# Kernel optimization log

Hardware: AMD Instinct MI355X
Metric: run time of the kernel (lower is better)

## Reference

```python
import jax, jax.numpy as jnp
import numpy as np

D = 64          # embed_dim == latent dim
T = 200         # diffusion_steps, timestep_respacing='' -> full 200 reverse steps
B, L = 8192, 100
N_ITEMS = 100000


def setup_inputs() -> dict:
    key = jax.random.key(0)
    ks = jax.random.split(key, 16)

    def lin(k, i, o):
        return (jax.random.normal(k, (i, o), jnp.float32) / np.sqrt(i)).astype(jnp.float32)

    item_seq = jax.random.randint(ks[0], (B, L), 0, N_ITEMS)
    item_emb = jax.random.normal(ks[1], (N_ITEMS, D), jnp.float32) * 0.02
    item_emb = item_emb.at[0].set(0.0)  # padding_idx=0
    return {
        'item_seq': item_seq,
        'item_emb': item_emb,
        'W_enc1': lin(ks[2], D, 256), 'b_enc1': jnp.zeros((256,), jnp.float32),
        'W_enc2': lin(ks[3], 256, 2 * D), 'b_enc2': jnp.zeros((2 * D,), jnp.float32),
        'W_in': lin(ks[4], D, D), 'b_in': jnp.zeros((D,), jnp.float32),
        'W_t': lin(ks[5], D, D), 'b_t': jnp.zeros((D,), jnp.float32),
        'W_c': lin(ks[6], D, D), 'b_c': jnp.zeros((D,), jnp.float32),
        'W_out': lin(ks[7], D, D), 'b_out': jnp.zeros((D,), jnp.float32),
    }


def _schedule():
    # improved-diffusion linear schedule
    scale = 1000.0 / T
    betas = jnp.linspace(scale * 1e-4, scale * 0.02, T, dtype=jnp.float32)
    alphas = 1.0 - betas
    acp = jnp.cumprod(alphas)
    acp_prev = jnp.concatenate([jnp.ones((1,), jnp.float32), acp[:-1]])
    sqrt_recip = jnp.sqrt(1.0 / acp)
    sqrt_recipm1 = jnp.sqrt(1.0 / acp - 1.0)
    post_var = betas * (1.0 - acp_prev) / (1.0 - acp)
    post_logvar = jnp.log(jnp.concatenate([post_var[1:2], post_var[1:]]))  # clipped
    coef1 = betas * jnp.sqrt(acp_prev) / (1.0 - acp)
    coef2 = (1.0 - acp_prev) * jnp.sqrt(alphas) / (1.0 - acp)
    return sqrt_recip, sqrt_recipm1, post_logvar, coef1, coef2


def reference(item_seq, item_emb, W_enc1, b_enc1, W_enc2, b_enc2,
              W_in, b_in, W_t, b_t, W_c, b_c, W_out, b_out):
    # ---- pooled VAE encoder (eval mode: dropout = identity, z = mu) ----
    seq = item_emb[item_seq]                                   # [B, L, D] gather
    cnt = jnp.sum(item_seq != 0, axis=1, keepdims=True).astype(seq.dtype)
    pooled = jnp.sum(seq, axis=1) / jnp.sqrt(cnt)              # [B, D]
    h = jax.nn.relu(pooled @ W_enc1 + b_enc1)
    enc = h @ W_enc2 + b_enc2                                  # [B, 2D]
    mu, logvar = jnp.split(enc, 2, axis=-1)
    z = mu                                                     # eval reparameterize

    # ---- ScoreNet: eps-prediction MLP conditioned on x_start and sinusoidal t ----
    half = D // 2
    freqs = jnp.exp(-jnp.log(10000.0) * jnp.arange(half, dtype=jnp.float32) / half)

    def scorenet(x, t_float, cond):
        ang = t_float * freqs                                  # [D/2]
        temb = jnp.concatenate([jnp.cos(ang), jnp.sin(ang)])   # [D]
        hh = jax.nn.silu(x @ W_in + b_in + (temb @ W_t + b_t) + cond @ W_c + b_c)
        return hh @ W_out + b_out                              # eps, [B, D]

    # ---- p_sample_loop (FIXED_SMALL variance, clip_denoised=True) ----
    sqrt_recip, sqrt_recipm1, post_logvar, coef1, coef2 = _schedule()
    x_init = jax.random.normal(jax.random.key(1), z.shape, z.dtype)
    noise_key = jax.random.key(2)

    def step(x, t):
        eps = scorenet(x, t.astype(jnp.float32), z)
        x0 = jnp.clip(sqrt_recip[t] * x - sqrt_recipm1[t] * eps, -1.0, 1.0)
        mean = coef1[t] * x0 + coef2[t] * x
        noise = jax.random.normal(jax.random.fold_in(noise_key, t), x.shape, x.dtype)
        sigma = jnp.where(t > 0, jnp.exp(0.5 * post_logvar[t]), 0.0)
        return mean + sigma * noise, None

    sample, _ = jax.lax.scan(step, x_init, jnp.arange(T - 1, -1, -1))
    return sample
```

## Files before the change

### kernel.cpp

```cpp
#include <hip/hip_runtime.h>
#include <cstdint>


#define DEVI __device__ __forceinline__

typedef __attribute__((ext_vector_type(8))) short short8;
typedef __attribute__((ext_vector_type(4))) float f32x4;

DEVI void threefry2x32(uint32_t k0, uint32_t k1, uint32_t x0, uint32_t x1,
                       uint32_t &o0, uint32_t &o1)
{
  const uint32_t ks2 = k0 ^ k1 ^ 0x1BD11BDAu;
  x0 += k0; x1 += k1;
#define TFR(r) { x0 += x1; x1 = __builtin_rotateleft32(x1, r); x1 ^= x0; }
  TFR(13u) TFR(15u) TFR(26u) TFR(6u)   x0 += k1;  x1 += ks2 + 1u;
  TFR(17u) TFR(29u) TFR(16u) TFR(24u)  x0 += ks2; x1 += k0 + 2u;
  TFR(13u) TFR(15u) TFR(26u) TFR(6u)   x0 += k0;  x1 += k1 + 3u;
  TFR(17u) TFR(29u) TFR(16u) TFR(24u)  x0 += k1;  x1 += ks2 + 4u;
  TFR(13u) TFR(15u) TFR(26u) TFR(6u)   x0 += ks2; x1 += k0 + 5u;
#undef TFR
  o0 = x0; o1 = x1;
}

DEVI uint32_t jax_random_bits32(uint32_t k0, uint32_t k1, uint32_t j)
{
  uint32_t a, b;
  threefry2x32(k0, k1, 0u, j, a, b);
  return a ^ b;
}

DEVI float jax_bits_to_normal(uint32_t bits)
{
  const float LO = -0.99999994f;
  float f = __uint_as_float((bits >> 9) | 0x3f800000u) - 1.0f;
  float u = fmaxf(LO, f * 2.0f + LO);
  float w = -__logf((1.0f - u) * (1.0f + u));
  float p;
  if (w < 5.0f) {
    w = w - 2.5f;
    p =              2.81022636e-08f;
    p = fmaf(p, w,   3.43273939e-07f);
    p = fmaf(p, w,  -3.5233877e-06f);
    p = fmaf(p, w,  -4.39150654e-06f);
    p = fmaf(p, w,   0.00021858087f);
    p = fmaf(p, w,  -0.00125372503f);
    p = fmaf(p, w,  -0.00417768164f);
    p = fmaf(p, w,   0.246640727f);
    p = fmaf(p, w,   1.50140941f);
  } else {
    w = sqrtf(w) - 3.0f;
    p =             -0.000200214257f;
    p = fmaf(p, w,   0.000100950558f);
    p = fmaf(p, w,   0.00134934322f);
    p = fmaf(p, w,  -0.00367342844f);
    p = fmaf(p, w,   0.00573950773f);
    p = fmaf(p, w,  -0.0076224613f);
    p = fmaf(p, w,   0.00943887047f);
    p = fmaf(p, w,   1.00167406f);
    p = fmaf(p, w,   2.83297682f);
  }
  return 1.41421356237f * (p * u);
}

DEVI short bf16_hi_trunc(float x) { return (short)(__float_as_uint(x) >> 16); }
DEVI float bf16_to_f32(short h)
{
  return __uint_as_float(((uint32_t)(unsigned short)h) << 16);
}
DEVI void split_bf16(float x, short &h, short &l)
{
  h = bf16_hi_trunc(x);
  float r = x - bf16_to_f32(h);
  l = bf16_hi_trunc(r);
}

DEVI short8 ld_frag16(const short* p)
{
  union { int4 v; short8 s; } u;
  u.v = *(const int4*)p;
  return u.s;
}

__global__ __launch_bounds__(256)
void k_poolprep(const int* __restrict__ seq, const float* __restrict__ emb,
                float* __restrict__ pooled,
                const float* __restrict__ Wt, const float* __restrict__ bt,
                const float* __restrict__ bin, float* __restrict__ tpb,
                float* __restrict__ sched)
{
  if (blockIdx.x < 2048u) {
    const int lane = threadIdx.x & 63;
    const int r    = blockIdx.x * 4 + (threadIdx.x >> 6);
    const int* row = seq + r * 100;
    float s = 0.f;
    int cnt = 0;
    for (int l = 0; l < 100; ++l) {
      int id = row[l];
      cnt += (id != 0);
      s += emb[id * 64 + lane];
    }
    pooled[r * 64 + lane] = s / sqrtf((float)cnt);
  } else {
    __shared__ float temb[64];
    const int t = blockIdx.x - 2048;
    const int d = threadIdx.x;
    if (d < 64) {
      const float lg = logf(10000.0f);
      int i = d & 31;
      float fr  = expf((-lg * (float)i) / 32.0f);
      float ang = (float)t * fr;
      temb[d] = (d < 32) ? cosf(ang) : sinf(ang);
      if (d == 0) {
        const float start = (float)(5.0 * 1e-4);
        const float stop  = (float)(5.0 * 0.02);
        const float delta = stop - start;
        float prod = 1.f, acp_prev = 1.f, beta = 0.f, alpha = 1.f;
        for (int i2 = 0; i2 <= t; ++i2) {
          beta  = start + ((float)i2 * delta) / 199.0f;
          alpha = 1.0f - beta;
          acp_prev = prod;
          prod = prod * alpha;
        }
        float acp = prod;
        float om  = 1.0f - acp;
        sched[t * 8 + 0] = sqrtf(1.0f / acp);
        sched[t * 8 + 1] = sqrtf(1.0f / acp - 1.0f);
        sched[t * 8 + 2] = beta * sqrtf(acp_prev) / om;
        sched[t * 8 + 3] = (1.0f - acp_prev) * sqrtf(alpha) / om;
        float pv = beta * (1.0f - acp_prev) / om;
        sched[t * 8 + 4] = (t > 0) ? sqrtf(pv) : 0.0f;
        uint32_t fk0, fk1;
        threefry2x32(0u, 2u, 0u, (uint32_t)t, fk0, fk1);
        ((uint32_t*)sched)[t * 8 + 5] = fk0;
        ((uint32_t*)sched)[t * 8 + 6] = fk1;
      }
    }
    __syncthreads();
    if (d < 64) {
      float acc = bt[d] + bin[d];
      for (int k = 0; k < 64; ++k)
        acc = fmaf(temb[k], Wt[k * 64 + d], acc);
      tpb[t * 64 + d] = acc;
    }
  }
}

__global__ __launch_bounds__(256)
void k_enc(const float* __restrict__ pooled,
           const float* __restrict__ W1, const float* __restrict__ b1,
           const float* __restrict__ W2, const float* __restrict__ b2,
           const float* __restrict__ Wc, const float* __restrict__ bc,
           float* __restrict__ cproj)
{
  __shared__ float p_s[8][64];
  __shared__ float h_s[8][256];
  __shared__ float mu_s[8][64];
  const int tid = threadIdx.x;
  const int r0  = blockIdx.x * 8;

  for (int i = tid; i < 8 * 64; i += 256)
    p_s[i >> 6][i & 63] = pooled[r0 * 64 + i];
  __syncthreads();

  float hacc[8];
#pragma unroll
  for (int r = 0; r < 8; ++r) hacc[r] = b1[tid];
  for (int k = 0; k < 64; ++k) {
    float w = W1[k * 256 + tid];
#pragma unroll
    for (int r = 0; r < 8; ++r) hacc[r] = fmaf(p_s[r][k], w, hacc[r]);
  }
#pragma unroll
  for (int r = 0; r < 8; ++r) h_s[r][tid] = fmaxf(hacc[r], 0.f);
  __syncthreads();

#pragma unroll
  for (int pass = 0; pass < 2; ++pass) {
    int r = pass * 4 + (tid >> 6);
    int j = tid & 63;
    float acc = b2[j];
    for (int k = 0; k < 256; ++k)
      acc = fmaf(h_s[r][k], W2[k * 128 + j], acc);
    mu_s[r][j] = acc;
  }
  __syncthreads();

#pragma unroll
  for (int pass = 0; pass < 2; ++pass) {
    int r = pass * 4 + (tid >> 6);
    int j = tid & 63;
    float acc = bc[j];
    for (int k = 0; k < 64; ++k)
      acc = fmaf(mu_s[r][k], Wc[k * 64 + j], acc);
    cproj[(r0 + r) * 64 + j] = acc;
  }
}

#define XLDW  72
#define NBW   68

__global__
__attribute__((amdgpu_flat_work_group_size(512, 512), amdgpu_waves_per_eu(4, 4)))
void k_ddpm(const float* __restrict__ Win, const float* __restrict__ Wout,
            const float* __restrict__ bout,
            const float* __restrict__ cproj, const float* __restrict__ tpb,
            const float* __restrict__ sched, float* __restrict__ out)
{
  __shared__ __align__(16) short Xh[16 * XLDW], Xl[16 * XLDW];
  __shared__ __align__(16) short Hh[16 * XLDW], Hl[16 * XLDW];
  __shared__ __align__(16) float nbuf[2 * 16 * NBW];

  const int tid  = threadIdx.x;
  const int lane = tid & 63;
  const int w    = tid >> 6;
  const bool gemv = (w < 4);
  const int r0g  = blockIdx.x * 16;
  const uint32_t* su = (const uint32_t*)sched;

  const int nt   = w & 3;
  const int nn   = lane & 15;
  const int quad = lane >> 4;
  const int dim  = nt * 16 + nn;
  const int arow = nn;
  const int kq0  = quad * 8;
  const int kq1  = 32 + quad * 8;
  const int rowb = quad * 4;

  const int cb   = w * 128 + lane * 2;
  const uint32_t jn = (uint32_t)(r0g * 64 + cb);
  const int nrow = cb >> 6;
  const int ndim = cb & 63;
  float* nb_w = &nbuf[nrow * NBW + ndim];

  short8 wiH0, wiL0, wiH1, wiL1, woH0, woL0, woH1, woL1;
  float cp[4] = {0.f, 0.f, 0.f, 0.f}, xo[4] = {0.f, 0.f, 0.f, 0.f};
  float bo = 0.f, tp = 0.f;
  uint32_t j0 = 0;

  if (gemv) {
#pragma unroll
    for (int j = 0; j < 8; ++j) {
      short h, l;
      split_bf16(Win[(kq0 + j) * 64 + dim], h, l);  wiH0[j] = h; wiL0[j] = l;
      split_bf16(Win[(kq1 + j) * 64 + dim], h, l);  wiH1[j] = h; wiL1[j] = l;
      split_bf16(Wout[(kq0 + j) * 64 + dim], h, l); woH0[j] = h; woL0[j] = l;
      split_bf16(Wout[(kq1 + j) * 64 + dim], h, l); woH1[j] = h; woL1[j] = l;
    }
    bo = bout[dim];
    j0 = (uint32_t)((r0g + rowb) * 64 + dim);
#pragma unroll
    for (int r = 0; r < 4; ++r) cp[r] = cproj[j0 + r * 64u];
#pragma unroll
    for (int r = 0; r < 4; ++r) {
      xo[r] = jax_bits_to_normal(jax_random_bits32(0u, 1u, j0 + r * 64u));
      short h, l;
      split_bf16(xo[r], h, l);
      Xh[(rowb + r) * XLDW + dim] = h; Xl[(rowb + r) * XLDW + dim] = l;
    }
    tp = tpb[199 * 64 + dim];
  }
  {
    const uint32_t fk0 = su[199 * 8 + 5];
    const uint32_t fk1 = su[199 * 8 + 6];
    float* d = nb_w + 16 * NBW;
    d[0] = jax_bits_to_normal(jax_random_bits32(fk0, fk1, jn + 0u));
    d[1] = jax_bits_to_normal(jax_random_bits32(fk0, fk1, jn + 1u));
  }
  __syncthreads();

#pragma unroll 1
  for (int t = 199; t >= 0; --t) {
    uint32_t gk0 = 0, gk1 = 0;
    float* nd = nullptr;
    if (t > 0) {
      gk0 = su[(t - 1) * 8 + 5];
      gk1 = su[(t - 1) * 8 + 6];
      nd = nb_w + ((t - 1) & 1) * 16 * NBW;
    }

    float sr = 0.f, srm1 = 0.f, c1 = 0.f, c2 = 0.f, sg = 0.f, tpn = 0.f;
    f32x4 acc;

    if (gemv) {
      sr   = sched[t * 8 + 0];
      srm1 = sched[t * 8 + 1];
      c1   = sched[t * 8 + 2];
      c2   = sched[t * 8 + 3];
      sg   = sched[t * 8 + 4];

#pragma unroll
      for (int r = 0; r < 4; ++r) acc[r] = tp + cp[r];
      {
        short8 xh0 = ld_frag16(&Xh[arow * XLDW + kq0]);
        short8 xl0 = ld_frag16(&Xl[arow * XLDW + kq0]);
        short8 xh1 = ld_frag16(&Xh[arow * XLDW + kq1]);
        short8 xl1 = ld_frag16(&Xl[arow * XLDW + kq1]);
        acc = __builtin_amdgcn_mfma_f32_16x16x32_bf16(xl0, wiH0, acc, 0, 0, 0);
        acc = __builtin_amdgcn_mfma_f32_16x16x32_bf16(xh0, wiL0, acc, 0, 0, 0);
        acc = __builtin_amdgcn_mfma_f32_16x16x32_bf16(xh0, wiH0, acc, 0, 0, 0);
        acc = __builtin_amdgcn_mfma_f32_16x16x32_bf16(xl1, wiH1, acc, 0, 0, 0);
        acc = __builtin_amdgcn_mfma_f32_16x16x32_bf16(xh1, wiL1, acc, 0, 0, 0);
        acc = __builtin_amdgcn_mfma_f32_16x16x32_bf16(xh1, wiH1, acc, 0, 0, 0);
      }
#pragma unroll
      for (int r = 0; r < 4; ++r) {
        float v = acc[r];
        v = v * __builtin_amdgcn_rcpf(1.0f + __expf(-v));
        short h, l;
        split_bf16(v, h, l);
        Hh[(rowb + r) * XLDW + dim] = h; Hl[(rowb + r) * XLDW + dim] = l;
      }
      int tn = (t > 0) ? (t - 1) : 0;
      tpn = tpb[tn * 64 + dim];
    }
    uint32_t b0 = 0, b1 = 0;
    if (t > 0) {
      b0 = jax_random_bits32(gk0, gk1, jn + 0u);
      b1 = jax_random_bits32(gk0, gk1, jn + 1u);
    }
    __syncthreads();

    if (gemv) {
      float n[4];
      const float* nr = &nbuf[(t & 1) * 16 * NBW + rowb * NBW + dim];
#pragma unroll
      for (int r = 0; r < 4; ++r) n[r] = nr[r * NBW];

      f32x4 eac;
#pragma unroll
      for (int r = 0; r < 4; ++r) eac[r] = bo;
      {
        short8 hh0 = ld_frag16(&Hh[arow * XLDW + kq0]);
        short8 hl0 = ld_frag16(&Hl[arow * XLDW + kq0]);
        short8 hh1 = ld_frag16(&Hh[arow * XLDW + kq1]);
        short8 hl1 = ld_frag16(&Hl[arow * XLDW + kq1]);
        eac = __builtin_amdgcn_mfma_f32_16x16x32_bf16(hl0, woH0, eac, 0, 0, 0);
        eac = __builtin_amdgcn_mfma_f32_16x16x32_bf16(hh0, woL0, eac, 0, 0, 0);
        eac = __builtin_amdgcn_mfma_f32_16x16x32_bf16(hh0, woH0, eac, 0, 0, 0);
        eac = __builtin_amdgcn_mfma_f32_16x16x32_bf16(hl1, woH1, eac, 0, 0, 0);
        eac = __builtin_amdgcn_mfma_f32_16x16x32_bf16(hh1, woL1, eac, 0, 0, 0);
        eac = __builtin_amdgcn_mfma_f32_16x16x32_bf16(hh1, woH1, eac, 0, 0, 0);
      }
#pragma unroll
      for (int r = 0; r < 4; ++r) {
        float xc = fminf(1.f, fmaxf(-1.f, sr * xo[r] - srm1 * eac[r]));
        xo[r] = c1 * xc + c2 * xo[r] + sg * n[r];
        short h, l;
        split_bf16(xo[r], h, l);
        Xh[(rowb + r) * XLDW + dim] = h; Xl[(rowb + r) * XLDW + dim] = l;
      }
      tp = tpn;
    }
    if (t > 0) {
      nd[0] = jax_bits_to_normal(b0);
      nd[1] = jax_bits_to_normal(b1);
    }
    __syncthreads();
  }

  if (gemv) {
#pragma unroll
    for (int r = 0; r < 4; ++r) out[j0 + r * 64u] = xo[r];
  }
}

extern "C" void kernel_launch(void* const* d_in, const int* in_sizes, int n_in,
                              void* d_out, int out_size, void* d_ws, size_t ws_size,
                              hipStream_t stream)
{
  const int*   seq  = (const int*)  d_in[0];
  const float* emb  = (const float*)d_in[1];
  const float* W1   = (const float*)d_in[2];
  const float* b1   = (const float*)d_in[3];
  const float* W2   = (const float*)d_in[4];
  const float* b2   = (const float*)d_in[5];
  const float* Win  = (const float*)d_in[6];
  const float* bin  = (const float*)d_in[7];
  const float* Wt   = (const float*)d_in[8];
  const float* bt   = (const float*)d_in[9];
  const float* Wc   = (const float*)d_in[10];
  const float* bc   = (const float*)d_in[11];
  const float* Wout = (const float*)d_in[12];
  const float* bout = (const float*)d_in[13];

  float* out   = (float*)d_out;
  float* ws    = (float*)d_ws;
  float* cproj = ws;
  float* tpb   = ws + 524288;
  float* sched = ws + 524288 + 12800;
  float* pooled = out;

  k_poolprep<<<2248, 256, 0, stream>>>(seq, emb, pooled, Wt, bt, bin, tpb, sched);
  k_enc  <<<1024, 256, 0, stream>>>(pooled, W1, b1, W2, b2, Wc, bc, cproj);
  k_ddpm <<<512, 512, 0, stream>>>(Win, Wout, bout, cproj, tpb, sched, out);
}
```

Measured before the change: 523.7 us.

## Split DDPM sampling into 4-row blocks with all waves computing

The sampling kernel now runs 2048 blocks of 256 threads, each handling 4 batch rows, instead of 512 blocks of 512 threads handling 16 rows. The old split had 4 MFMA waves and 4 waves that only produced noise. Now every wave does both MFMA GEMV work and noise generation, and each thread produces one noise value per step instead of two. The 16-row MFMA tiles are zero-padded, with only 4 live rows stored. This trades a fourfold increase in wasted MFMA work for more resident waves per CU and a shorter per-step dependency chain, to hide latency in the 200-step serial loop.

Result: slower. 759.3 us (+45.0%).

```diff
diff --git a/kernel.cpp b/kernel.cpp
--- a/kernel.cpp
+++ b/kernel.cpp
@@ -200,7 +200,7 @@
 #define NBW   68
 
 __global__
-__attribute__((amdgpu_flat_work_group_size(512, 512), amdgpu_waves_per_eu(4, 4)))
+__attribute__((amdgpu_flat_work_group_size(256, 256), amdgpu_waves_per_eu(4, 8)))
 void k_ddpm(const float* __restrict__ Win, const float* __restrict__ Wout,
             const float* __restrict__ bout,
             const float* __restrict__ cproj, const float* __restrict__ tpb,
@@ -208,46 +208,47 @@
 {
   __shared__ __align__(16) short Xh[16 * XLDW], Xl[16 * XLDW];
   __shared__ __align__(16) short Hh[16 * XLDW], Hl[16 * XLDW];
-  __shared__ __align__(16) float nbuf[2 * 16 * NBW];
+  __shared__ __align__(16) float nbuf[2 * 4 * NBW];
 
   const int tid  = threadIdx.x;
   const int lane = tid & 63;
   const int w    = tid >> 6;
-  const bool gemv = (w < 4);
-  const int r0g  = blockIdx.x * 16;
+  const int r0g  = blockIdx.x * 4;
   const uint32_t* su = (const uint32_t*)sched;
 
-  const int nt   = w & 3;
   const int nn   = lane & 15;
   const int quad = lane >> 4;
-  const int dim  = nt * 16 + nn;
+  const int dim  = w * 16 + nn;
   const int arow = nn;
   const int kq0  = quad * 8;
   const int kq1  = 32 + quad * 8;
-  const int rowb = quad * 4;
-
-  const int cb   = w * 128 + lane * 2;
+  const bool own = (quad == 0);
+
+  const int cb   = w * 64 + lane;
   const uint32_t jn = (uint32_t)(r0g * 64 + cb);
   const int nrow = cb >> 6;
   const int ndim = cb & 63;
   float* nb_w = &nbuf[nrow * NBW + ndim];
 
+  for (int i = tid; i < 16 * XLDW; i += 256) {
+    Xh[i] = 0; Xl[i] = 0; Hh[i] = 0; Hl[i] = 0;
+  }
+
   short8 wiH0, wiL0, wiH1, wiL1, woH0, woL0, woH1, woL1;
+#pragma unroll
+  for (int j = 0; j < 8; ++j) {
+    short h, l;
+    split_bf16(Win[(kq0 + j) * 64 + dim], h, l);  wiH0[j] = h; wiL0[j] = l;
+    split_bf16(Win[(kq1 + j) * 64 + dim], h, l);  wiH1[j] = h; wiL1[j] = l;
+    split_bf16(Wout[(kq0 + j) * 64 + dim], h, l); woH0[j] = h; woL0[j] = l;
+    split_bf16(Wout[(kq1 + j) * 64 + dim], h, l); woH1[j] = h; woL1[j] = l;
+  }
+
+  const float bo = bout[dim];
+  const uint32_t j0 = (uint32_t)(r0g * 64 + dim);
   float cp[4] = {0.f, 0.f, 0.f, 0.f}, xo[4] = {0.f, 0.f, 0.f, 0.f};
-  float bo = 0.f, tp = 0.f;
-  uint32_t j0 = 0;
-
-  if (gemv) {
-#pragma unroll
-    for (int j = 0; j < 8; ++j) {
-      short h, l;
-      split_bf16(Win[(kq0 + j) * 64 + dim], h, l);  wiH0[j] = h; wiL0[j] = l;
-      split_bf16(Win[(kq1 + j) * 64 + dim], h, l);  wiH1[j] = h; wiL1[j] = l;
-      split_bf16(Wout[(kq0 + j) * 64 + dim], h, l); woH0[j] = h; woL0[j] = l;
-      split_bf16(Wout[(kq1 + j) * 64 + dim], h, l); woH1[j] = h; woL1[j] = l;
-    }
-    bo = bout[dim];
-    j0 = (uint32_t)((r0g + rowb) * 64 + dim);
+
+  if (own) {
 #pragma unroll
     for (int r = 0; r < 4; ++r) cp[r] = cproj[j0 + r * 64u];
 #pragma unroll
@@ -255,16 +256,15 @@
       xo[r] = jax_bits_to_normal(jax_random_bits32(0u, 1u, j0 + r * 64u));
       short h, l;
       split_bf16(xo[r], h, l);
-      Xh[(rowb + r) * XLDW + dim] = h; Xl[(rowb + r) * XLDW + dim] = l;
-    }
-    tp = tpb[199 * 64 + dim];
-  }
+      Xh[r * XLDW + dim] = h; Xl[r * XLDW + dim] = l;
+    }
+  }
+  float tp = tpb[199 * 64 + dim];
+
   {
     const uint32_t fk0 = su[199 * 8 + 5];
     const uint32_t fk1 = su[199 * 8 + 6];
-    float* d = nb_w + 16 * NBW;
-    d[0] = jax_bits_to_normal(jax_random_bits32(fk0, fk1, jn + 0u));
-    d[1] = jax_bits_to_normal(jax_random_bits32(fk0, fk1, jn + 1u));
+    nb_w[4 * NBW] = jax_bits_to_normal(jax_random_bits32(fk0, fk1, jn));
   }
   __syncthreads();
 
@@ -275,56 +275,52 @@
     if (t > 0) {
       gk0 = su[(t - 1) * 8 + 5];
       gk1 = su[(t - 1) * 8 + 6];
-      nd = nb_w + ((t - 1) & 1) * 16 * NBW;
-    }
-
-    float sr = 0.f, srm1 = 0.f, c1 = 0.f, c2 = 0.f, sg = 0.f, tpn = 0.f;
+      nd = nb_w + ((t - 1) & 1) * 4 * NBW;
+    }
+
+    const float sr   = sched[t * 8 + 0];
+    const float srm1 = sched[t * 8 + 1];
+    const float c1   = sched[t * 8 + 2];
+    const float c2   = sched[t * 8 + 3];
+    const float sg   = sched[t * 8 + 4];
+
     f32x4 acc;
-
-    if (gemv) {
-      sr   = sched[t * 8 + 0];
-      srm1 = sched[t * 8 + 1];
-      c1   = sched[t * 8 + 2];
-      c2   = sched[t * 8 + 3];
-      sg   = sched[t * 8 + 4];
-
-#pragma unroll
-      for (int r = 0; r < 4; ++r) acc[r] = tp + cp[r];
-      {
-        short8 xh0 = ld_frag16(&Xh[arow * XLDW + kq0]);
-        short8 xl0 = ld_frag16(&Xl[arow * XLDW + kq0]);
-        short8 xh1 = ld_frag16(&Xh[arow * XLDW + kq1]);
-        short8 xl1 = ld_frag16(&Xl[arow * XLDW + kq1]);
-        acc = __builtin_amdgcn_mfma_f32_16x16x32_bf16(xl0, wiH0, acc, 0, 0, 0);
-        acc = __builtin_amdgcn_mfma_f32_16x16x32_bf16(xh0, wiL0, acc, 0, 0, 0);
-        acc = __builtin_amdgcn_mfma_f32_16x16x32_bf16(xh0, wiH0, acc, 0, 0, 0);
-        acc = __builtin_amdgcn_mfma_f32_16x16x32_bf16(xl1, wiH1, acc, 0, 0, 0);
-        acc = __builtin_amdgcn_mfma_f32_16x16x32_bf16(xh1, wiL1, acc, 0, 0, 0);
-        acc = __builtin_amdgcn_mfma_f32_16x16x32_bf16(xh1, wiH1, acc, 0, 0, 0);
-      }
+#pragma unroll
+    for (int r = 0; r < 4; ++r) acc[r] = tp + cp[r];
+    {
+      short8 xh0 = ld_frag16(&Xh[arow * XLDW + kq0]);
+      short8 xl0 = ld_frag16(&Xl[arow * XLDW + kq0]);
+      short8 xh1 = ld_frag16(&Xh[arow * XLDW + kq1]);
+      short8 xl1 = ld_frag16(&Xl[arow * XLDW + kq1]);
+      acc = __builtin_amdgcn_mfma_f32_16x16x32_bf16(xl0, wiH0, acc, 0, 0, 0);
+      acc = __builtin_amdgcn_mfma_f32_16x16x32_bf16(xh0, wiL0, acc, 0, 0, 0);
+      acc = __builtin_amdgcn_mfma_f32_16x16x32_bf16(xh0, wiH0, acc, 0, 0, 0);
+      acc = __builtin_amdgcn_mfma_f32_16x16x32_bf16(xl1, wiH1, acc, 0, 0, 0);
+      acc = __builtin_amdgcn_mfma_f32_16x16x32_bf16(xh1, wiL1, acc, 0, 0, 0);
+      acc = __builtin_amdgcn_mfma_f32_16x16x32_bf16(xh1, wiH1, acc, 0, 0, 0);
+    }
+    if (own) {
 #pragma unroll
       for (int r = 0; r < 4; ++r) {
         float v = acc[r];
         v = v * __builtin_amdgcn_rcpf(1.0f + __expf(-v));
         short h, l;
         split_bf16(v, h, l);
-        Hh[(rowb + r) * XLDW + dim] = h; Hl[(rowb + r) * XLDW + dim] = l;
+        Hh[r * XLDW + dim] = h; Hl[r * XLDW + dim] = l;
       }
-      int tn = (t > 0) ? (t - 1) : 0;
-      tpn = tpb[tn * 64 + dim];
-    }
-    uint32_t b0 = 0, b1 = 0;
-    if (t > 0) {
-      b0 = jax_random_bits32(gk0, gk1, jn + 0u);
-      b1 = jax_random_bits32(gk0, gk1, jn + 1u);
-    }
+    }
+    int tn = (t > 0) ? (t - 1) : 0;
+    float tpn = tpb[tn * 64 + dim];
+
+    uint32_t b0 = 0;
+    if (t > 0) b0 = jax_random_bits32(gk0, gk1, jn);
     __syncthreads();
 
-    if (gemv) {
+    {
       float n[4];
-      const float* nr = &nbuf[(t & 1) * 16 * NBW + rowb * NBW + dim];
-#pragma unroll
-      for (int r = 0; r < 4; ++r) n[r] = nr[r * NBW];
+#pragma unroll
+      for (int r = 0; r < 4; ++r)
+        n[r] = nbuf[(t & 1) * 4 * NBW + r * NBW + dim];
 
       f32x4 eac;
 #pragma unroll
@@ -341,24 +337,23 @@
         eac = __builtin_amdgcn_mfma_f32_16x16x32_bf16(hh1, woL1, eac, 0, 0, 0);
         eac = __builtin_amdgcn_mfma_f32_16x16x32_bf16(hh1, woH1, eac, 0, 0, 0);
       }
-#pragma unroll
-      for (int r = 0; r < 4; ++r) {
-        float xc = fminf(1.f, fmaxf(-1.f, sr * xo[r] - srm1 * eac[r]));
-        xo[r] = c1 * xc + c2 * xo[r] + sg * n[r];
-        short h, l;
-        split_bf16(xo[r], h, l);
-        Xh[(rowb + r) * XLDW + dim] = h; Xl[(rowb + r) * XLDW + dim] = l;
+      if (own) {
+#pragma unroll
+        for (int r = 0; r < 4; ++r) {
+          float xc = fminf(1.f, fmaxf(-1.f, sr * xo[r] - srm1 * eac[r]));
+          xo[r] = c1 * xc + c2 * xo[r] + sg * n[r];
+          short h, l;
+          split_bf16(xo[r], h, l);
+          Xh[r * XLDW + dim] = h; Xl[r * XLDW + dim] = l;
+        }
       }
       tp = tpn;
     }
-    if (t > 0) {
-      nd[0] = jax_bits_to_normal(b0);
-      nd[1] = jax_bits_to_normal(b1);
-    }
+    if (t > 0) nd[0] = jax_bits_to_normal(b0);
     __syncthreads();
   }
 
-  if (gemv) {
+  if (own) {
 #pragma unroll
     for (int r = 0; r < 4; ++r) out[j0 + r * 64u] = xo[r];
   }
@@ -392,5 +387,5 @@
 
   k_poolprep<<<2248, 256, 0, stream>>>(seq, emb, pooled, Wt, bt, bin, tpb, sched);
   k_enc  <<<1024, 256, 0, stream>>>(pooled, W1, b1, W2, b2, Wc, bc, cproj);
-  k_ddpm <<<512, 512, 0, stream>>>(Win, Wout, bout, cproj, tpb, sched, out);
-}
+  k_ddpm <<<2048, 256, 0, stream>>>(Win, Wout, bout, cproj, tpb, sched, out);
+}
```
